# Optimization experiments

Measured on AMD Instinct MI355X. Metric: run time of the kernel, lower is better.

Reference implementation:

```python
import jax, jax.numpy as jnp
import numpy as np

N = 50000   # nodes
E = 600000  # edges per relation
H = 4       # heads
DH = 32     # head dim (out_feat // num_heads)
D = 128     # in_feat == out_feat
NEG_SLOPE = 0.2


def setup_inputs() -> dict:
    key = jax.random.key(0)
    ks = jax.random.split(key, 13)
    x = jax.random.normal(ks[0], (N, D), jnp.float32)
    src_r0 = jax.random.randint(ks[1], (E,), 0, N, jnp.int32)
    dst_r0 = jax.random.randint(ks[2], (E,), 0, N, jnp.int32)
    src_r1 = jax.random.randint(ks[3], (E,), 0, N, jnp.int32)
    dst_r1 = jax.random.randint(ks[4], (E,), 0, N, jnp.int32)
    s = 0.05  # keep activations moderate (xavier-like scale)
    W_r0 = jax.random.normal(ks[5], (D, H * DH), jnp.float32) * s
    attn_l_r0 = jax.random.normal(ks[6], (H, DH), jnp.float32) * s
    attn_r_r0 = jax.random.normal(ks[7], (H, DH), jnp.float32) * s
    W_r1 = jax.random.normal(ks[8], (D, H * DH), jnp.float32) * s
    attn_l_r1 = jax.random.normal(ks[9], (H, DH), jnp.float32) * s
    attn_r_r1 = jax.random.normal(ks[10], (H, DH), jnp.float32) * s
    loop_weight = jax.random.normal(ks[11], (D, D), jnp.float32) * s
    h_bias = jnp.zeros((D,), jnp.float32)
    return {"x": x, "src_r0": src_r0, "dst_r0": dst_r0, "src_r1": src_r1,
            "dst_r1": dst_r1, "W_r0": W_r0, "attn_l_r0": attn_l_r0,
            "attn_r_r0": attn_r_r0, "W_r1": W_r1, "attn_l_r1": attn_l_r1,
            "attn_r_r1": attn_r_r1, "loop_weight": loop_weight, "h_bias": h_bias}


def _gat_rel(x, src, dst, W, attn_l, attn_r):
    """DGL GATConv for one relation: fc -> per-node attn scalars -> edge
    leaky_relu -> per-dst softmax -> weighted scatter-sum. Heads flattened."""
    feat = (x @ W).reshape(-1, H, DH)                 # [N, H, DH]
    el = jnp.einsum('nhd,hd->nh', feat, attn_l)       # [N, H]
    er = jnp.einsum('nhd,hd->nh', feat, attn_r)       # [N, H]
    e = jax.nn.leaky_relu(el[src] + er[dst], NEG_SLOPE)  # [E, H]
    # edge softmax per destination node, per head (numerically stable)
    m = jax.ops.segment_max(e, dst, num_segments=N)   # [N, H]
    ex = jnp.exp(e - m[dst])                          # [E, H]
    z = jax.ops.segment_sum(ex, dst, num_segments=N)  # [N, H]
    a = ex / z[dst]                                   # [E, H]
    msg = a[:, :, None] * feat[src]                   # [E, H, DH]
    out = jax.ops.segment_sum(msg, dst, num_segments=N)  # [N, H, DH]
    return out.reshape(-1, H * DH)                    # [N, D] (concat heads)


def reference(x, src_r0, dst_r0, src_r1, dst_r1, W_r0, attn_l_r0, attn_r_r0,
              W_r1, attn_l_r1, attn_r_r1, loop_weight, h_bias):
    # HeteroGraphConv with default 'sum' aggregation across relations
    h = _gat_rel(x, src_r0, dst_r0, W_r0, attn_l_r0, attn_r_r0)
    h = h + _gat_rel(x, src_r1, dst_r1, W_r1, attn_l_r1, attn_r_r1)
    # self-loop linear + bias + activation (dropout p=0.0 is identity)
    h = h + x @ loop_weight + h_bias
    return jax.nn.relu(h)
```

## Files before the change

kernel.cpp:

```cpp
#include <hip/hip_runtime.h>
#include <math.h>


#define CAP 48
#define NB 256
#define BCAP 2752
#define BIN_EDGES 8192

typedef __attribute__((ext_vector_type(8))) short short8v;
typedef __attribute__((ext_vector_type(4))) float float4v;

__device__ __forceinline__ unsigned short f2bf(float f) {
  unsigned int u = __float_as_uint(f);
  unsigned int r = (u + 0x7fffu + ((u >> 16) & 1u)) >> 16;
  return (unsigned short)r;
}
__device__ __forceinline__ float2 bfpair(unsigned int u) {
  float2 r;
  r.x = __uint_as_float(u << 16);
  r.y = __uint_as_float(u & 0xffff0000u);
  return r;
}

__global__ __launch_bounds__(512) void prep_bin_kernel(
    const float* __restrict__ W0, const float* __restrict__ W1,
    const float* __restrict__ WL,
    const float* __restrict__ al0, const float* __restrict__ ar0,
    const float* __restrict__ al1, const float* __restrict__ ar1,
    const int* __restrict__ src0, const int* __restrict__ dst0,
    const int* __restrict__ src1, const int* __restrict__ dst1,
    unsigned short* __restrict__ Wtall,
    unsigned int* __restrict__ bpair, int* __restrict__ gcnt,
    int E, int width, int nconvb, int nbin)
{
  __shared__ int smem[512];
  const int t = threadIdx.x;

  if ((int)blockIdx.x < nconvb) {
    const int j = blockIdx.x * 512 + t;
    if (j < 4096) {
      const int rel = j >> 11;
      const int q = j & 2047;
      const int n = q >> 4;
      const int k0 = (q & 15) * 8;
      const float* W = rel ? W1 : W0;
      unsigned short o[8];
#pragma unroll
      for (int u = 0; u < 8; ++u) o[u] = f2bf(W[(size_t)(k0 + u) * 128 + n]);
      *(short8v*)&Wtall[(size_t)rel * 18432 + n * 128 + k0] = *(short8v*)o;
    } else if (j < 4352) {
      const int e = j - 4096;
      const int rel = e >> 7;
      const int q = e & 127;
      const int cIdx = q >> 4;
      const int isr = cIdx >> 2;
      const int h = cIdx & 3;
      const int k0 = (q & 15) * 8;
      const float* W = rel ? W1 : W0;
      const float* av = isr ? (rel ? ar1 : ar0) : (rel ? al1 : al0);
      unsigned short o[8];
#pragma unroll
      for (int u = 0; u < 8; ++u) {
        float s = 0.f;
#pragma unroll
        for (int d = 0; d < 32; ++d)
          s += W[(size_t)(k0 + u) * 128 + h * 32 + d] * av[h * 32 + d];
        o[u] = f2bf(s);
      }
      *(short8v*)&Wtall[(size_t)rel * 18432 + (128 + cIdx) * 128 + k0] = *(short8v*)o;
    } else if (j < 4608) {
      const int e = j - 4352;
      const int rel = e >> 7;
      const int q = e & 127;
      const int cIdx = 136 + (q >> 4);
      const int k0 = (q & 15) * 8;
      const short8v z = {0,0,0,0,0,0,0,0};
      *(short8v*)&Wtall[(size_t)rel * 18432 + cIdx * 128 + k0] = z;
    } else if (j < 6656) {
      const int e = j - 4608;
      const int n = e >> 4;
      const int k0 = (e & 15) * 8;
      unsigned short o[8];
#pragma unroll
      for (int u = 0; u < 8; ++u) o[u] = f2bf(WL[(size_t)(k0 + u) * 128 + n]);
      *(short8v*)&Wtall[(size_t)2 * 18432 + n * 128 + k0] = *(short8v*)o;
    }
  } else {
    int* cnt = smem;
    int* gb  = smem + NB;
    const int bid = blockIdx.x - nconvb;
    const int rel = (bid >= nbin) ? 1 : 0;
    const int ib  = rel ? (bid - nbin) : bid;
    const int* srcA = rel ? src1 : src0;
    const int* dstA = rel ? dst1 : dst0;
    const int base = ib * BIN_EDGES;
    const int cntE = min(E - base, BIN_EDGES);

    for (int i = t; i < NB; i += 512) cnt[i] = 0;
    __syncthreads();

    unsigned int epack[16]; int eb[16], epos[16];
#pragma unroll
    for (int q = 0; q < 16; ++q) {
      const int ei = q * 512 + t;
      if (ei < cntE) {
        const int s = srcA[base + ei];
        const int d = dstA[base + ei];
        const int b = d / width;
        const int ld = d - b * width;
        epack[q] = (unsigned int)s | ((unsigned int)ld << 16);
        eb[q] = b;
        epos[q] = atomicAdd(&cnt[b], 1);
      } else {
        eb[q] = -1;
      }
    }
    __syncthreads();
    for (int i = t; i < NB; i += 512)
      gb[i] = atomicAdd(&gcnt[rel * NB + i], cnt[i]);
    __syncthreads();
#pragma unroll
    for (int q = 0; q < 16; ++q) {
      if (eb[q] >= 0) {
        const int slot = gb[eb[q]] + epos[q];
        if (slot < BCAP)
          bpair[(size_t)(rel * NB + eb[q]) * BCAP + slot] = epack[q];
      }
    }
  }
}

__global__ __launch_bounds__(256) void gemm_ell_kernel(
    const float* __restrict__ x, const unsigned short* __restrict__ Wtall,
    unsigned short* __restrict__ f0, unsigned short* __restrict__ f1,
    unsigned short* __restrict__ xl,
    float* __restrict__ el0, float* __restrict__ er0,
    float* __restrict__ el1, float* __restrict__ er1,
    const unsigned int* __restrict__ bpair, const int* __restrict__ gcnt,
    int* __restrict__ deg, unsigned short* __restrict__ ell0,
    unsigned short* __restrict__ ell1,
    int N, int width, int ngemm)
{
  __shared__ int ldeg[256];

  if ((int)blockIdx.x < ngemm) {
    const int wave = threadIdx.x >> 6, lane = threadIdx.x & 63;
    const int lr = lane & 15, lk = lane >> 4;
    const int row0 = blockIdx.x * 128 + wave * 32;

    short8v a[2][4];
#pragma unroll
    for (int mf = 0; mf < 2; ++mf) {
      const int r = row0 + mf * 16 + lr;
#pragma unroll
      for (int kc = 0; kc < 4; ++kc) {
        if (r < N) {
          const float* xp = &x[(size_t)r * 128 + kc * 32 + lk * 8];
          float4 u = *(const float4*)xp;
          float4 v = *(const float4*)(xp + 4);
          unsigned short o[8];
          o[0]=f2bf(u.x); o[1]=f2bf(u.y); o[2]=f2bf(u.z); o[3]=f2bf(u.w);
          o[4]=f2bf(v.x); o[5]=f2bf(v.y); o[6]=f2bf(v.z); o[7]=f2bf(v.w);
          a[mf][kc] = *(short8v*)o;
        } else {
          a[mf][kc] = (short8v){0,0,0,0,0,0,0,0};
        }
      }
    }

#pragma unroll
    for (int w = 0; w < 3; ++w) {
      const unsigned short* Wp = Wtall + (size_t)w * 18432;
      const int NF = (w < 2) ? 9 : 8;
      float4v acc[2][9];
#pragma unroll
      for (int mf = 0; mf < 2; ++mf)
#pragma unroll
        for (int nf = 0; nf < 9; ++nf) acc[mf][nf] = (float4v){0.f, 0.f, 0.f, 0.f};
      for (int nf = 0; nf < NF; ++nf) {
        const unsigned short* Bp = &Wp[(size_t)(nf * 16 + lr) * 128];
#pragma unroll
        for (int kc = 0; kc < 4; ++kc) {
          const short8v b = *(const short8v*)&Bp[kc * 32 + lk * 8];
          acc[0][nf] = __builtin_amdgcn_mfma_f32_16x16x32_bf16(a[0][kc], b, acc[0][nf], 0, 0, 0);
          acc[1][nf] = __builtin_amdgcn_mfma_f32_16x16x32_bf16(a[1][kc], b, acc[1][nf], 0, 0, 0);
        }
      }

      unsigned short* dstp = (w == 0) ? f0 : (w == 1) ? f1 : xl;
#pragma unroll
      for (int mf = 0; mf < 2; ++mf) {
#pragma unroll
        for (int nf = 0; nf < 8; ++nf) {
          const int col = nf * 16 + lr;
#pragma unroll
          for (int j = 0; j < 4; ++j) {
            const int row = row0 + mf * 16 + lk * 4 + j;
            if (row < N) dstp[(size_t)row * 128 + col] = f2bf(acc[mf][nf][j]);
          }
        }
      }
      if (w < 2 && lr < 8) {
        float* ep = (lr < 4) ? (w ? el1 : el0) : (w ? er1 : er0);
        const int h = lr & 3;
#pragma unroll
        for (int mf = 0; mf < 2; ++mf)
#pragma unroll
          for (int j = 0; j < 4; ++j) {
            const int row = row0 + mf * 16 + lk * 4 + j;
            if (row < N) ep[row * 4 + h] = acc[mf][8][j];
          }
      }
    }
  } else {
    const int bid = blockIdx.x - ngemm;
    const int rel = bid >> 8;
    const int b = bid & 255;
    const int t = threadIdx.x;
    const int d0 = b * width;
    if (t < width) ldeg[t] = 0;
    __syncthreads();
    const int count = min(gcnt[rel * NB + b], BCAP);
    unsigned short* ell = rel ? ell1 : ell0;
    const unsigned int* bp = &bpair[(size_t)(rel * NB + b) * BCAP];
    for (int i = t; i < count; i += 256) {
      const unsigned int v = bp[i];
      const int src = (int)(v & 0xFFFFu);
      const int ld = (int)(v >> 16);
      const int slot = atomicAdd(&ldeg[ld], 1);
      if (slot < CAP) ell[(size_t)(d0 + ld) * CAP + slot] = (unsigned short)src;
    }
    __syncthreads();
    if (t < width && d0 + t < N) deg[rel * N + d0 + t] = ldeg[t];
  }
}

__global__ __launch_bounds__(256) void gat_aggregate_kernel(
    const unsigned short* __restrict__ f0, const unsigned short* __restrict__ f1,
    const unsigned short* __restrict__ xl,
    const float* __restrict__ el0, const float* __restrict__ er0,
    const float* __restrict__ el1, const float* __restrict__ er1,
    const int* __restrict__ deg,
    const unsigned short* __restrict__ ell0, const unsigned short* __restrict__ ell1,
    const float* __restrict__ bias, float* __restrict__ out, int N)
{
  __shared__ float p_lds[4][2][4][16];
  const int wid  = threadIdx.x >> 6;
  const int lane = threadIdx.x & 63;
  const int n = blockIdx.x * 4 + wid;
  if (n >= N) return;
  const int h  = lane >> 4;
  const int il = lane & 15;
  const int c  = lane * 2;

  const int rs0 = (int)ell0[(size_t)n * CAP + il];
  const int rs1 = (int)ell1[(size_t)n * CAP + il];
  const int d0 = min(deg[n], CAP);
  const int d1 = min(deg[N + n], CAP);
  const float er0h = er0[n * 4 + h];
  const float er1h = er1[n * 4 + h];

  const bool v0 = il < d0, v1 = il < d1;
  const int s0 = v0 ? rs0 : 0;
  const int s1 = v1 ? rs1 : 0;
  const float elv0 = el0[s0 * 4 + h];
  const float elv1 = el1[s1 * 4 + h];

  float m0, sum0, m1, sum1;
  {
    float e = elv0 + er0h;  e = e > 0.f ? e : 0.2f * e;
    float ev = v0 ? e : -INFINITY;
    float cm = ev;
    cm = fmaxf(cm, __shfl_xor(cm, 1)); cm = fmaxf(cm, __shfl_xor(cm, 2));
    cm = fmaxf(cm, __shfl_xor(cm, 4)); cm = fmaxf(cm, __shfl_xor(cm, 8));
    const float p = __expf(ev - cm);
    float cs = p;
    cs += __shfl_xor(cs, 1); cs += __shfl_xor(cs, 2);
    cs += __shfl_xor(cs, 4); cs += __shfl_xor(cs, 8);
    m0 = cm; sum0 = cs;
    p_lds[wid][0][h][il] = p;
  }
  {
    float e = elv1 + er1h;  e = e > 0.f ? e : 0.2f * e;
    float ev = v1 ? e : -INFINITY;
    float cm = ev;
    cm = fmaxf(cm, __shfl_xor(cm, 1)); cm = fmaxf(cm, __shfl_xor(cm, 2));
    cm = fmaxf(cm, __shfl_xor(cm, 4)); cm = fmaxf(cm, __shfl_xor(cm, 8));
    const float p = __expf(ev - cm);
    float cs = p;
    cs += __shfl_xor(cs, 1); cs += __shfl_xor(cs, 2);
    cs += __shfl_xor(cs, 4); cs += __shfl_xor(cs, 8);
    m1 = cm; sum1 = cs;
    p_lds[wid][1][h][il] = p;
  }

  unsigned int fu0[16], fu1[16];
#pragma unroll
  for (int i = 0; i < 16; ++i) {
    const int s = __builtin_amdgcn_readlane(s0, i);
    fu0[i] = *(const unsigned int*)&f0[(size_t)s * 128 + c];
  }
#pragma unroll
  for (int i = 0; i < 16; ++i) {
    const int s = __builtin_amdgcn_readlane(s1, i);
    fu1[i] = *(const unsigned int*)&f1[(size_t)s * 128 + c];
  }

  float ax0 = 0.f, ay0 = 0.f;
  {
    float p16[16];
    *(float4*)&p16[0]  = *(const float4*)&p_lds[wid][0][h][0];
    *(float4*)&p16[4]  = *(const float4*)&p_lds[wid][0][h][4];
    *(float4*)&p16[8]  = *(const float4*)&p_lds[wid][0][h][8];
    *(float4*)&p16[12] = *(const float4*)&p_lds[wid][0][h][12];
    float axa=0.f, aya=0.f, axb=0.f, ayb=0.f;
#pragma unroll
    for (int i = 0; i < 16; i += 2) {
      const float2 fa = bfpair(fu0[i]);
      const float2 fb2 = bfpair(fu0[i+1]);
      axa += p16[i]*fa.x;   aya += p16[i]*fa.y;
      axb += p16[i+1]*fb2.x; ayb += p16[i+1]*fb2.y;
    }
    ax0 = axa + axb; ay0 = aya + ayb;
  }
  float ax1 = 0.f, ay1 = 0.f;
  {
    float p16[16];
    *(float4*)&p16[0]  = *(const float4*)&p_lds[wid][1][h][0];
    *(float4*)&p16[4]  = *(const float4*)&p_lds[wid][1][h][4];
    *(float4*)&p16[8]  = *(const float4*)&p_lds[wid][1][h][8];
    *(float4*)&p16[12] = *(const float4*)&p_lds[wid][1][h][12];
    float axa=0.f, aya=0.f, axb=0.f, ayb=0.f;
#pragma unroll
    for (int i = 0; i < 16; i += 2) {
      const float2 fa = bfpair(fu1[i]);
      const float2 fb2 = bfpair(fu1[i+1]);
      axa += p16[i]*fa.x;   aya += p16[i]*fa.y;
      axb += p16[i+1]*fb2.x; ayb += p16[i+1]*fb2.y;
    }
    ax1 = axa + axb; ay1 = aya + ayb;
  }

  auto tail = [&](const unsigned short* ellp, const float* elp, float erh,
                  int d, const unsigned short* fbp, float& m, float& sum,
                  float& ax, float& ay, int slot) {
    for (int base = 16; base < d; base += 16) {
      const bool valid = (base + il) < d;
      int sv = (int)ellp[(size_t)n * CAP + base + il];
      sv = valid ? sv : 0;
      const float elv = elp[sv * 4 + h];
      float e = elv + erh; e = e > 0.f ? e : 0.2f * e;
      const float ev = valid ? e : -INFINITY;
      float cm = ev;
      cm = fmaxf(cm, __shfl_xor(cm, 1)); cm = fmaxf(cm, __shfl_xor(cm, 2));
      cm = fmaxf(cm, __shfl_xor(cm, 4)); cm = fmaxf(cm, __shfl_xor(cm, 8));
      const float mn = fmaxf(m, cm);
      const float scale = __expf(m - mn);
      const float p = __expf(ev - mn);
      float cs = p;
      cs += __shfl_xor(cs, 1); cs += __shfl_xor(cs, 2);
      cs += __shfl_xor(cs, 4); cs += __shfl_xor(cs, 8);
      sum = sum * scale + cs;
      m = mn;
      p_lds[wid][slot][h][il] = p;
      unsigned int fu[16];
#pragma unroll
      for (int i = 0; i < 16; ++i) {
        const int s = __builtin_amdgcn_readlane(sv, i);
        fu[i] = *(const unsigned int*)&fbp[(size_t)s * 128 + c];
      }
      float p16[16];
      *(float4*)&p16[0]  = *(const float4*)&p_lds[wid][slot][h][0];
      *(float4*)&p16[4]  = *(const float4*)&p_lds[wid][slot][h][4];
      *(float4*)&p16[8]  = *(const float4*)&p_lds[wid][slot][h][8];
      *(float4*)&p16[12] = *(const float4*)&p_lds[wid][slot][h][12];
      float axa=0.f, aya=0.f;
#pragma unroll
      for (int i = 0; i < 16; ++i) {
        const float2 f = bfpair(fu[i]);
        axa += p16[i]*f.x; aya += p16[i]*f.y;
      }
      ax = ax * scale + axa;
      ay = ay * scale + aya;
    }
  };
  if (d0 > 16) tail(ell0, el0, er0h, d0, f0, m0, sum0, ax0, ay0, 0);
  if (d1 > 16) tail(ell1, el1, er1h, d1, f1, m1, sum1, ax1, ay1, 1);

  float ox = 0.f, oy = 0.f;
  if (d0 > 0) { const float inv = 1.f / sum0; ox += ax0 * inv; oy += ay0 * inv; }
  if (d1 > 0) { const float inv = 1.f / sum1; ox += ax1 * inv; oy += ay1 * inv; }
  const float2 xlv = bfpair(*(const unsigned int*)&xl[(size_t)n * 128 + c]);
  const float2 bv  = *(const float2*)&bias[c];
  ox += xlv.x + bv.x;
  oy += xlv.y + bv.y;
  float2 res;
  res.x = fmaxf(ox, 0.f);
  res.y = fmaxf(oy, 0.f);
  *(float2*)&out[(size_t)n * 128 + c] = res;
}

extern "C" void kernel_launch(void* const* d_in, const int* in_sizes, int n_in,
                              void* d_out, int out_size, void* d_ws, size_t ws_size,
                              hipStream_t stream)
{
  const int N = in_sizes[0] / 128;
  const int E = in_sizes[1];

  const float* x    = (const float*)d_in[0];
  const int* src0   = (const int*)d_in[1];
  const int* dst0   = (const int*)d_in[2];
  const int* src1   = (const int*)d_in[3];
  const int* dst1   = (const int*)d_in[4];
  const float* W0   = (const float*)d_in[5];
  const float* al0  = (const float*)d_in[6];
  const float* ar0  = (const float*)d_in[7];
  const float* W1   = (const float*)d_in[8];
  const float* al1  = (const float*)d_in[9];
  const float* ar1  = (const float*)d_in[10];
  const float* WL   = (const float*)d_in[11];
  const float* bias = (const float*)d_in[12];
  float* out = (float*)d_out;

  char* p = (char*)d_ws;
  auto alloc = [&](size_t bytes) { char* r = p; p += (bytes + 255) & ~(size_t)255; return r; };
  unsigned short* f0 = (unsigned short*)alloc((size_t)N * 128 * 2);
  unsigned short* f1 = (unsigned short*)alloc((size_t)N * 128 * 2);
  unsigned short* xl = (unsigned short*)alloc((size_t)N * 128 * 2);
  float* el0 = (float*)alloc((size_t)N * 4 * 4);
  float* er0 = (float*)alloc((size_t)N * 4 * 4);
  float* el1 = (float*)alloc((size_t)N * 4 * 4);
  float* er1 = (float*)alloc((size_t)N * 4 * 4);
  int* deg   = (int*)alloc((size_t)2 * N * 4);
  unsigned short* ell0 = (unsigned short*)alloc((size_t)CAP * N * 2);
  unsigned short* ell1 = (unsigned short*)alloc((size_t)CAP * N * 2);
  unsigned int* bpair = (unsigned int*)alloc((size_t)2 * NB * BCAP * 4);
  int* gcnt  = (int*)alloc((size_t)2 * NB * 4);
  unsigned short* Wtall = (unsigned short*)alloc((size_t)(2 * 144 + 128) * 128 * 2);

  const int width = (N + NB - 1) / NB;
  const int ngemm = (N + 127) / 128;
  const int nbin  = (E + BIN_EDGES - 1) / BIN_EDGES;
  const int nconvb = 13;

  hipMemsetAsync(gcnt, 0, (size_t)2 * NB * 4, stream);

  prep_bin_kernel<<<nconvb + 2 * nbin, 512, 0, stream>>>(
      W0, W1, WL, al0, ar0, al1, ar1, src0, dst0, src1, dst1,
      Wtall, bpair, gcnt, E, width, nconvb, nbin);

  gemm_ell_kernel<<<ngemm + 2 * NB, 256, 0, stream>>>(
      x, Wtall, f0, f1, xl, el0, er0, el1, er1,
      bpair, gcnt, deg, ell0, ell1, N, width, ngemm);

  gat_aggregate_kernel<<<(N + 3) / 4, 256, 0, stream>>>(
      f0, f1, xl, el0, er0, el1, er1, deg, ell0, ell1, bias, out, N);
}
```

Before: 128.9 us.

## Co-schedule edge binning with GEMM, split ELL build, two nodes per wave

```diff
diff --git a/kernel.cpp b/kernel.cpp
--- a/kernel.cpp
+++ b/kernel.cpp
@@ -5,7 +5,7 @@
 #define CAP 48
 #define NB 256
 #define BCAP 2752
-#define BIN_EDGES 8192
+#define BIN_EDGES 4096
 
 typedef __attribute__((ext_vector_type(8))) short short8v;
 typedef __attribute__((ext_vector_type(4))) float float4v;
@@ -22,126 +22,80 @@
   return r;
 }
 
-__global__ __launch_bounds__(512) void prep_bin_kernel(
+__global__ __launch_bounds__(256) void prep_kernel(
     const float* __restrict__ W0, const float* __restrict__ W1,
     const float* __restrict__ WL,
     const float* __restrict__ al0, const float* __restrict__ ar0,
     const float* __restrict__ al1, const float* __restrict__ ar1,
+    unsigned short* __restrict__ Wtall, int* __restrict__ gcnt)
+{
+  const int t = threadIdx.x;
+  if (blockIdx.x == 0) {
+    gcnt[t] = 0;
+    gcnt[t + 256] = 0;
+  }
+  const int j = blockIdx.x * 256 + t;
+  if (j < 4096) {
+    const int rel = j >> 11;
+    const int q = j & 2047;
+    const int n = q >> 4;
+    const int k0 = (q & 15) * 8;
+    const float* W = rel ? W1 : W0;
+    unsigned short o[8];
+#pragma unroll
+    for (int u = 0; u < 8; ++u) o[u] = f2bf(W[(size_t)(k0 + u) * 128 + n]);
+    *(short8v*)&Wtall[(size_t)rel * 18432 + n * 128 + k0] = *(short8v*)o;
+  } else if (j < 4352) {
+    const int e = j - 4096;
+    const int rel = e >> 7;
+    const int q = e & 127;
+    const int cIdx = q >> 4;
+    const int isr = cIdx >> 2;
+    const int h = cIdx & 3;
+    const int k0 = (q & 15) * 8;
+    const float* W = rel ? W1 : W0;
+    const float* av = isr ? (rel ? ar1 : ar0) : (rel ? al1 : al0);
+    unsigned short o[8];
+#pragma unroll
+    for (int u = 0; u < 8; ++u) {
+      float s = 0.f;
+#pragma unroll
+      for (int d = 0; d < 32; ++d)
+        s += W[(size_t)(k0 + u) * 128 + h * 32 + d] * av[h * 32 + d];
+      o[u] = f2bf(s);
+    }
+    *(short8v*)&Wtall[(size_t)rel * 18432 + (128 + cIdx) * 128 + k0] = *(short8v*)o;
+  } else if (j < 4608) {
+    const int e = j - 4352;
+    const int rel = e >> 7;
+    const int q = e & 127;
+    const int cIdx = 136 + (q >> 4);
+    const int k0 = (q & 15) * 8;
+    const short8v z = {0,0,0,0,0,0,0,0};
+    *(short8v*)&Wtall[(size_t)rel * 18432 + cIdx * 128 + k0] = z;
+  } else if (j < 6656) {
+    const int e = j - 4608;
+    const int n = e >> 4;
+    const int k0 = (e & 15) * 8;
+    unsigned short o[8];
+#pragma unroll
+    for (int u = 0; u < 8; ++u) o[u] = f2bf(WL[(size_t)(k0 + u) * 128 + n]);
+    *(short8v*)&Wtall[(size_t)2 * 18432 + n * 128 + k0] = *(short8v*)o;
+  }
+}
+
+__global__ __launch_bounds__(256) void gemm_bin_kernel(
+    const float* __restrict__ x, const unsigned short* __restrict__ Wtall,
     const int* __restrict__ src0, const int* __restrict__ dst0,
     const int* __restrict__ src1, const int* __restrict__ dst1,
-    unsigned short* __restrict__ Wtall,
-    unsigned int* __restrict__ bpair, int* __restrict__ gcnt,
-    int E, int width, int nconvb, int nbin)
-{
-  __shared__ int smem[512];
-  const int t = threadIdx.x;
-
-  if ((int)blockIdx.x < nconvb) {
-    const int j = blockIdx.x * 512 + t;
-    if (j < 4096) {
-      const int rel = j >> 11;
-      const int q = j & 2047;
-      const int n = q >> 4;
-      const int k0 = (q & 15) * 8;
-      const float* W = rel ? W1 : W0;
-      unsigned short o[8];
-#pragma unroll
-      for (int u = 0; u < 8; ++u) o[u] = f2bf(W[(size_t)(k0 + u) * 128 + n]);
-      *(short8v*)&Wtall[(size_t)rel * 18432 + n * 128 + k0] = *(short8v*)o;
-    } else if (j < 4352) {
-      const int e = j - 4096;
-      const int rel = e >> 7;
-      const int q = e & 127;
-      const int cIdx = q >> 4;
-      const int isr = cIdx >> 2;
-      const int h = cIdx & 3;
-      const int k0 = (q & 15) * 8;
-      const float* W = rel ? W1 : W0;
-      const float* av = isr ? (rel ? ar1 : ar0) : (rel ? al1 : al0);
-      unsigned short o[8];
-#pragma unroll
-      for (int u = 0; u < 8; ++u) {
-        float s = 0.f;
-#pragma unroll
-        for (int d = 0; d < 32; ++d)
-          s += W[(size_t)(k0 + u) * 128 + h * 32 + d] * av[h * 32 + d];
-        o[u] = f2bf(s);
-      }
-      *(short8v*)&Wtall[(size_t)rel * 18432 + (128 + cIdx) * 128 + k0] = *(short8v*)o;
-    } else if (j < 4608) {
-      const int e = j - 4352;
-      const int rel = e >> 7;
-      const int q = e & 127;
-      const int cIdx = 136 + (q >> 4);
-      const int k0 = (q & 15) * 8;
-      const short8v z = {0,0,0,0,0,0,0,0};
-      *(short8v*)&Wtall[(size_t)rel * 18432 + cIdx * 128 + k0] = z;
-    } else if (j < 6656) {
-      const int e = j - 4608;
-      const int n = e >> 4;
-      const int k0 = (e & 15) * 8;
-      unsigned short o[8];
-#pragma unroll
-      for (int u = 0; u < 8; ++u) o[u] = f2bf(WL[(size_t)(k0 + u) * 128 + n]);
-      *(short8v*)&Wtall[(size_t)2 * 18432 + n * 128 + k0] = *(short8v*)o;
-    }
-  } else {
-    int* cnt = smem;
-    int* gb  = smem + NB;
-    const int bid = blockIdx.x - nconvb;
-    const int rel = (bid >= nbin) ? 1 : 0;
-    const int ib  = rel ? (bid - nbin) : bid;
-    const int* srcA = rel ? src1 : src0;
-    const int* dstA = rel ? dst1 : dst0;
-    const int base = ib * BIN_EDGES;
-    const int cntE = min(E - base, BIN_EDGES);
-
-    for (int i = t; i < NB; i += 512) cnt[i] = 0;
-    __syncthreads();
-
-    unsigned int epack[16]; int eb[16], epos[16];
-#pragma unroll
-    for (int q = 0; q < 16; ++q) {
-      const int ei = q * 512 + t;
-      if (ei < cntE) {
-        const int s = srcA[base + ei];
-        const int d = dstA[base + ei];
-        const int b = d / width;
-        const int ld = d - b * width;
-        epack[q] = (unsigned int)s | ((unsigned int)ld << 16);
-        eb[q] = b;
-        epos[q] = atomicAdd(&cnt[b], 1);
-      } else {
-        eb[q] = -1;
-      }
-    }
-    __syncthreads();
-    for (int i = t; i < NB; i += 512)
-      gb[i] = atomicAdd(&gcnt[rel * NB + i], cnt[i]);
-    __syncthreads();
-#pragma unroll
-    for (int q = 0; q < 16; ++q) {
-      if (eb[q] >= 0) {
-        const int slot = gb[eb[q]] + epos[q];
-        if (slot < BCAP)
-          bpair[(size_t)(rel * NB + eb[q]) * BCAP + slot] = epack[q];
-      }
-    }
-  }
-}
-
-__global__ __launch_bounds__(256) void gemm_ell_kernel(
-    const float* __restrict__ x, const unsigned short* __restrict__ Wtall,
     unsigned short* __restrict__ f0, unsigned short* __restrict__ f1,
     unsigned short* __restrict__ xl,
     float* __restrict__ el0, float* __restrict__ er0,
     float* __restrict__ el1, float* __restrict__ er1,
-    const unsigned int* __restrict__ bpair, const int* __restrict__ gcnt,
-    int* __restrict__ deg, unsigned short* __restrict__ ell0,
-    unsigned short* __restrict__ ell1,
-    int N, int width, int ngemm)
+    unsigned int* __restrict__ bpair, int* __restrict__ gcnt,
+    int N, int E, int width, int ngemm, int nbin)
 {
-  __shared__ int ldeg[256];
+  __shared__ int smem[512];
 
   if ((int)blockIdx.x < ngemm) {
     const int wave = threadIdx.x >> 6, lane = threadIdx.x & 63;
@@ -213,26 +167,74 @@
       }
     }
   } else {
+    int* cnt = smem;
+    int* gb  = smem + NB;
+    const int t = threadIdx.x;
     const int bid = blockIdx.x - ngemm;
-    const int rel = bid >> 8;
-    const int b = bid & 255;
-    const int t = threadIdx.x;
-    const int d0 = b * width;
-    if (t < width) ldeg[t] = 0;
+    const int rel = (bid >= nbin) ? 1 : 0;
+    const int ib  = rel ? (bid - nbin) : bid;
+    const int* srcA = rel ? src1 : src0;
+    const int* dstA = rel ? dst1 : dst0;
+    const int base = ib * BIN_EDGES;
+    const int cntE = min(E - base, BIN_EDGES);
+
+    cnt[t] = 0;
     __syncthreads();
-    const int count = min(gcnt[rel * NB + b], BCAP);
-    unsigned short* ell = rel ? ell1 : ell0;
-    const unsigned int* bp = &bpair[(size_t)(rel * NB + b) * BCAP];
-    for (int i = t; i < count; i += 256) {
-      const unsigned int v = bp[i];
-      const int src = (int)(v & 0xFFFFu);
-      const int ld = (int)(v >> 16);
-      const int slot = atomicAdd(&ldeg[ld], 1);
-      if (slot < CAP) ell[(size_t)(d0 + ld) * CAP + slot] = (unsigned short)src;
+
+    unsigned int epack[16]; int eb[16], epos[16];
+#pragma unroll
+    for (int q = 0; q < 16; ++q) {
+      const int ei = q * 256 + t;
+      if (ei < cntE) {
+        const int s = srcA[base + ei];
+        const int d = dstA[base + ei];
+        const int b = d / width;
+        const int ld = d - b * width;
+        epack[q] = (unsigned int)s | ((unsigned int)ld << 16);
+        eb[q] = b;
+        epos[q] = atomicAdd(&cnt[b], 1);
+      } else {
+        eb[q] = -1;
+      }
     }
     __syncthreads();
-    if (t < width && d0 + t < N) deg[rel * N + d0 + t] = ldeg[t];
+    gb[t] = atomicAdd(&gcnt[rel * NB + t], cnt[t]);
+    __syncthreads();
+#pragma unroll
+    for (int q = 0; q < 16; ++q) {
+      if (eb[q] >= 0) {
+        const int slot = gb[eb[q]] + epos[q];
+        if (slot < BCAP)
+          bpair[(size_t)(rel * NB + eb[q]) * BCAP + slot] = epack[q];
+      }
+    }
   }
+}
+
+__global__ __launch_bounds__(256) void ell_build_kernel(
+    const unsigned int* __restrict__ bpair, const int* __restrict__ gcnt,
+    int* __restrict__ deg, unsigned short* __restrict__ ell0,
+    unsigned short* __restrict__ ell1, int N, int width)
+{
+  __shared__ int ldeg[256];
+  const int rel = blockIdx.x >> 8;
+  const int b = blockIdx.x & 255;
+  const int t = threadIdx.x;
+  const int d0 = b * width;
+  if (t < width) ldeg[t] = 0;
+  __syncthreads();
+  const int count = min(gcnt[rel * NB + b], BCAP);
+  unsigned short* ell = rel ? ell1 : ell0;
+  const unsigned int* bp = &bpair[(size_t)(rel * NB + b) * BCAP];
+  for (int i = t; i < count; i += 256) {
+    const unsigned int v = bp[i];
+    const int src = (int)(v & 0xFFFFu);
+    const int ld = (int)(v >> 16);
+    const int slot = atomicAdd(&ldeg[ld], 1);
+    if (slot < CAP) ell[(size_t)(d0 + ld) * CAP + slot] = (unsigned short)src;
+  }
+  __syncthreads();
+  if (t < width && d0 + t < N) deg[rel * N + d0 + t] = ldeg[t];
 }
 
 __global__ __launch_bounds__(256) void gat_aggregate_kernel(
@@ -247,157 +249,171 @@
   __shared__ float p_lds[4][2][4][16];
   const int wid  = threadIdx.x >> 6;
   const int lane = threadIdx.x & 63;
-  const int n = blockIdx.x * 4 + wid;
-  if (n >= N) return;
   const int h  = lane >> 4;
   const int il = lane & 15;
   const int c  = lane * 2;
-
-  const int rs0 = (int)ell0[(size_t)n * CAP + il];
-  const int rs1 = (int)ell1[(size_t)n * CAP + il];
-  const int d0 = min(deg[n], CAP);
-  const int d1 = min(deg[N + n], CAP);
-  const float er0h = er0[n * 4 + h];
-  const float er1h = er1[n * 4 + h];
-
-  const bool v0 = il < d0, v1 = il < d1;
-  const int s0 = v0 ? rs0 : 0;
-  const int s1 = v1 ? rs1 : 0;
-  const float elv0 = el0[s0 * 4 + h];
-  const float elv1 = el1[s1 * 4 + h];
-
-  float m0, sum0, m1, sum1;
-  {
-    float e = elv0 + er0h;  e = e > 0.f ? e : 0.2f * e;
-    float ev = v0 ? e : -INFINITY;
-    float cm = ev;
-    cm = fmaxf(cm, __shfl_xor(cm, 1)); cm = fmaxf(cm, __shfl_xor(cm, 2));
-    cm = fmaxf(cm, __shfl_xor(cm, 4)); cm = fmaxf(cm, __shfl_xor(cm, 8));
-    const float p = __expf(ev - cm);
-    float cs = p;
-    cs += __shfl_xor(cs, 1); cs += __shfl_xor(cs, 2);
-    cs += __shfl_xor(cs, 4); cs += __shfl_xor(cs, 8);
-    m0 = cm; sum0 = cs;
-    p_lds[wid][0][h][il] = p;
-  }
-  {
-    float e = elv1 + er1h;  e = e > 0.f ? e : 0.2f * e;
-    float ev = v1 ? e : -INFINITY;
-    float cm = ev;
-    cm = fmaxf(cm, __shfl_xor(cm, 1)); cm = fmaxf(cm, __shfl_xor(cm, 2));
-    cm = fmaxf(cm, __shfl_xor(cm, 4)); cm = fmaxf(cm, __shfl_xor(cm, 8));
-    const float p = __expf(ev - cm);
-    float cs = p;
-    cs += __shfl_xor(cs, 1); cs += __shfl_xor(cs, 2);
-    cs += __shfl_xor(cs, 4); cs += __shfl_xor(cs, 8);
-    m1 = cm; sum1 = cs;
-    p_lds[wid][1][h][il] = p;
-  }
-
-  unsigned int fu0[16], fu1[16];
-#pragma unroll
-  for (int i = 0; i < 16; ++i) {
-    const int s = __builtin_amdgcn_readlane(s0, i);
-    fu0[i] = *(const unsigned int*)&f0[(size_t)s * 128 + c];
-  }
-#pragma unroll
-  for (int i = 0; i < 16; ++i) {
-    const int s = __builtin_amdgcn_readlane(s1, i);
-    fu1[i] = *(const unsigned int*)&f1[(size_t)s * 128 + c];
-  }
-
-  float ax0 = 0.f, ay0 = 0.f;
-  {
-    float p16[16];
-    *(float4*)&p16[0]  = *(const float4*)&p_lds[wid][0][h][0];
-    *(float4*)&p16[4]  = *(const float4*)&p_lds[wid][0][h][4];
-    *(float4*)&p16[8]  = *(const float4*)&p_lds[wid][0][h][8];
-    *(float4*)&p16[12] = *(const float4*)&p_lds[wid][0][h][12];
-    float axa=0.f, aya=0.f, axb=0.f, ayb=0.f;
-#pragma unroll
-    for (int i = 0; i < 16; i += 2) {
-      const float2 fa = bfpair(fu0[i]);
-      const float2 fb2 = bfpair(fu0[i+1]);
-      axa += p16[i]*fa.x;   aya += p16[i]*fa.y;
-      axb += p16[i+1]*fb2.x; ayb += p16[i+1]*fb2.y;
-    }
-    ax0 = axa + axb; ay0 = aya + ayb;
-  }
-  float ax1 = 0.f, ay1 = 0.f;
-  {
-    float p16[16];
-    *(float4*)&p16[0]  = *(const float4*)&p_lds[wid][1][h][0];
-    *(float4*)&p16[4]  = *(const float4*)&p_lds[wid][1][h][4];
-    *(float4*)&p16[8]  = *(const float4*)&p_lds[wid][1][h][8];
-    *(float4*)&p16[12] = *(const float4*)&p_lds[wid][1][h][12];
-    float axa=0.f, aya=0.f, axb=0.f, ayb=0.f;
-#pragma unroll
-    for (int i = 0; i < 16; i += 2) {
-      const float2 fa = bfpair(fu1[i]);
-      const float2 fb2 = bfpair(fu1[i+1]);
-      axa += p16[i]*fa.x;   aya += p16[i]*fa.y;
-      axb += p16[i+1]*fb2.x; ayb += p16[i+1]*fb2.y;
-    }
-    ax1 = axa + axb; ay1 = aya + ayb;
-  }
-
-  auto tail = [&](const unsigned short* ellp, const float* elp, float erh,
-                  int d, const unsigned short* fbp, float& m, float& sum,
-                  float& ax, float& ay, int slot) {
-    for (int base = 16; base < d; base += 16) {
-      const bool valid = (base + il) < d;
-      int sv = (int)ellp[(size_t)n * CAP + base + il];
-      sv = valid ? sv : 0;
-      const float elv = elp[sv * 4 + h];
-      float e = elv + erh; e = e > 0.f ? e : 0.2f * e;
-      const float ev = valid ? e : -INFINITY;
+  const int n0 = (blockIdx.x * 4 + wid) * 2;
+  if (n0 >= N) return;
+  const bool actB = (n0 + 1) < N;
+  const int nA = n0, nB = actB ? (n0 + 1) : n0;
+
+  const int rA0 = (int)ell0[(size_t)nA * CAP + il];
+  const int rA1 = (int)ell1[(size_t)nA * CAP + il];
+  const int rB0 = (int)ell0[(size_t)nB * CAP + il];
+  const int rB1 = (int)ell1[(size_t)nB * CAP + il];
+  const int dA0 = min(deg[nA], CAP),     dA1 = min(deg[N + nA], CAP);
+  const int dB0 = actB ? min(deg[nB], CAP) : 0;
+  const int dB1 = actB ? min(deg[N + nB], CAP) : 0;
+  const float erA0 = er0[nA * 4 + h], erA1 = er1[nA * 4 + h];
+  const float erB0 = er0[nB * 4 + h], erB1 = er1[nB * 4 + h];
+
+  const int sA0 = (il < dA0) ? rA0 : 0;
+  const int sA1 = (il < dA1) ? rA1 : 0;
+  const int sB0 = (il < dB0) ? rB0 : 0;
+  const int sB1 = (il < dB1) ? rB1 : 0;
+
+  const float elA0 = el0[sA0 * 4 + h];
+  const float elA1 = el1[sA1 * 4 + h];
+  const float elB0 = el0[sB0 * 4 + h];
+  const float elB1 = el1[sB1 * 4 + h];
+
+  auto process = [&](int n, int s0, int s1, int d0, int d1,
+                     float er0h, float er1h, float elv0, float elv1) {
+    float m0, sum0, m1, sum1;
+    {
+      float e = elv0 + er0h;  e = e > 0.f ? e : 0.2f * e;
+      float ev = (il < d0) ? e : -INFINITY;
       float cm = ev;
       cm = fmaxf(cm, __shfl_xor(cm, 1)); cm = fmaxf(cm, __shfl_xor(cm, 2));
       cm = fmaxf(cm, __shfl_xor(cm, 4)); cm = fmaxf(cm, __shfl_xor(cm, 8));
-      const float mn = fmaxf(m, cm);
-      const float scale = __expf(m - mn);
-      const float p = __expf(ev - mn);
+      const float p = __expf(ev - cm);
       float cs = p;
       cs += __shfl_xor(cs, 1); cs += __shfl_xor(cs, 2);
       cs += __shfl_xor(cs, 4); cs += __shfl_xor(cs, 8);
-      sum = sum * scale + cs;
-      m = mn;
-      p_lds[wid][slot][h][il] = p;
-      unsigned int fu[16];
-#pragma unroll
-      for (int i = 0; i < 16; ++i) {
-        const int s = __builtin_amdgcn_readlane(sv, i);
-        fu[i] = *(const unsigned int*)&fbp[(size_t)s * 128 + c];
-      }
+      m0 = cm; sum0 = cs;
+      p_lds[wid][0][h][il] = p;
+    }
+    {
+      float e = elv1 + er1h;  e = e > 0.f ? e : 0.2f * e;
+      float ev = (il < d1) ? e : -INFINITY;
+      float cm = ev;
+      cm = fmaxf(cm, __shfl_xor(cm, 1)); cm = fmaxf(cm, __shfl_xor(cm, 2));
+      cm = fmaxf(cm, __shfl_xor(cm, 4)); cm = fmaxf(cm, __shfl_xor(cm, 8));
+      const float p = __expf(ev - cm);
+      float cs = p;
+      cs += __shfl_xor(cs, 1); cs += __shfl_xor(cs, 2);
+      cs += __shfl_xor(cs, 4); cs += __shfl_xor(cs, 8);
+      m1 = cm; sum1 = cs;
+      p_lds[wid][1][h][il] = p;
+    }
+
+    unsigned int fu0[16], fu1[16];
+#pragma unroll
+    for (int i = 0; i < 16; ++i) {
+      const int s = __builtin_amdgcn_readlane(s0, i);
+      fu0[i] = *(const unsigned int*)&f0[(size_t)s * 128 + c];
+    }
+#pragma unroll
+    for (int i = 0; i < 16; ++i) {
+      const int s = __builtin_amdgcn_readlane(s1, i);
+      fu1[i] = *(const unsigned int*)&f1[(size_t)s * 128 + c];
+    }
+
+    float ax0, ay0, ax1, ay1;
+    {
       float p16[16];
-      *(float4*)&p16[0]  = *(const float4*)&p_lds[wid][slot][h][0];
-      *(float4*)&p16[4]  = *(const float4*)&p_lds[wid][slot][h][4];
-      *(float4*)&p16[8]  = *(const float4*)&p_lds[wid][slot][h][8];
-      *(float4*)&p16[12] = *(const float4*)&p_lds[wid][slot][h][12];
-      float axa=0.f, aya=0.f;
-#pragma unroll
-      for (int i = 0; i < 16; ++i) {
-        const float2 f = bfpair(fu[i]);
-        axa += p16[i]*f.x; aya += p16[i]*f.y;
-      }
-      ax = ax * scale + axa;
-      ay = ay * scale + aya;
-    }
+      *(float4*)&p16[0]  = *(const float4*)&p_lds[wid][0][h][0];
+      *(float4*)&p16[4]  = *(const float4*)&p_lds[wid][0][h][4];
+      *(float4*)&p16[8]  = *(const float4*)&p_lds[wid][0][h][8];
+      *(float4*)&p16[12] = *(const float4*)&p_lds[wid][0][h][12];
+      float axa=0.f, aya=0.f, axb=0.f, ayb=0.f;
+#pragma unroll
+      for (int i = 0; i < 16; i += 2) {
+        const float2 fa = bfpair(fu0[i]);
+        const float2 fb2 = bfpair(fu0[i+1]);
+        axa += p16[i]*fa.x;   aya += p16[i]*fa.y;
+        axb += p16[i+1]*fb2.x; ayb += p16[i+1]*fb2.y;
+      }
+      ax0 = axa + axb; ay0 = aya + ayb;
+    }
+    {
+      float p16[16];
+      *(float4*)&p16[0]  = *(const float4*)&p_lds[wid][1][h][0];
+      *(float4*)&p16[4]  = *(const float4*)&p_lds[wid][1][h][4];
+      *(float4*)&p16[8]  = *(const float4*)&p_lds[wid][1][h][8];
+      *(float4*)&p16[12] = *(const float4*)&p_lds[wid][1][h][12];
+      float axa=0.f, aya=0.f, axb=0.f, ayb=0.f;
+#pragma unroll
+      for (int i = 0; i < 16; i += 2) {
+        const float2 fa = bfpair(fu1[i]);
+        const float2 fb2 = bfpair(fu1[i+1]);
+        axa += p16[i]*fa.x;   aya += p16[i]*fa.y;
+        axb += p16[i+1]*fb2.x; ayb += p16[i+1]*fb2.y;
+      }
+      ax1 = axa + axb; ay1 = aya + ayb;
+    }
+
+    auto tail = [&](const unsigned short* ellp, const float* elp, float erh,
+                    int d, const unsigned short* fbp, float& m, float& sum,
+                    float& ax, float& ay, int slot) {
+      for (int base = 16; base < d; base += 16) {
+        const bool valid = (base + il) < d;
+        int sv = (int)ellp[(size_t)n * CAP + base + il];
+        sv = valid ? sv : 0;
+        const float elv = elp[sv * 4 + h];
+        float e = elv + erh; e = e > 0.f ? e : 0.2f * e;
+        const float ev = valid ? e : -INFINITY;
+        float cm = ev;
+        cm = fmaxf(cm, __shfl_xor(cm, 1)); cm = fmaxf(cm, __shfl_xor(cm, 2));
+        cm = fmaxf(cm, __shfl_xor(cm, 4)); cm = fmaxf(cm, __shfl_xor(cm, 8));
+        const float mn = fmaxf(m, cm);
+        const float scale = __expf(m - mn);
+        const float p = __expf(ev - mn);
+        float cs = p;
+        cs += __shfl_xor(cs, 1); cs += __shfl_xor(cs, 2);
+        cs += __shfl_xor(cs, 4); cs += __shfl_xor(cs, 8);
+        sum = sum * scale + cs;
+        m = mn;
+        p_lds[wid][slot][h][il] = p;
+        unsigned int fu[16];
+#pragma unroll
+        for (int i = 0; i < 16; ++i) {
+          const int s = __builtin_amdgcn_readlane(sv, i);
+          fu[i] = *(const unsigned int*)&fbp[(size_t)s * 128 + c];
+        }
+        float p16[16];
+        *(float4*)&p16[0]  = *(const float4*)&p_lds[wid][slot][h][0];
+        *(float4*)&p16[4]  = *(const float4*)&p_lds[wid][slot][h][4];
+        *(float4*)&p16[8]  = *(const float4*)&p_lds[wid][slot][h][8];
+        *(float4*)&p16[12] = *(const float4*)&p_lds[wid][slot][h][12];
+        float axa=0.f, aya=0.f;
+#pragma unroll
+        for (int i = 0; i < 16; ++i) {
+          const float2 f = bfpair(fu[i]);
+          axa += p16[i]*f.x; aya += p16[i]*f.y;
+        }
+        ax = ax * scale + axa;
+        ay = ay * scale + aya;
+      }
+    };
+    if (d0 > 16) tail(ell0, el0, er0h, d0, f0, m0, sum0, ax0, ay0, 0);
+    if (d1 > 16) tail(ell1, el1, er1h, d1, f1, m1, sum1, ax1, ay1, 1);
+
+    float ox = 0.f, oy = 0.f;
+    if (d0 > 0) { const float inv = 1.f / sum0; ox += ax0 * inv; oy += ay0 * inv; }
+    if (d1 > 0) { const float inv = 1.f / sum1; ox += ax1 * inv; oy += ay1 * inv; }
+    const float2 xlv = bfpair(*(const unsigned int*)&xl[(size_t)n * 128 + c]);
+    const float2 bv  = *(const float2*)&bias[c];
+    ox += xlv.x + bv.x;
+    oy += xlv.y + bv.y;
+    float2 res;
+    res.x = fmaxf(ox, 0.f);
+    res.y = fmaxf(oy, 0.f);
+    *(float2*)&out[(size_t)n * 128 + c] = res;
   };
-  if (d0 > 16) tail(ell0, el0, er0h, d0, f0, m0, sum0, ax0, ay0, 0);
-  if (d1 > 16) tail(ell1, el1, er1h, d1, f1, m1, sum1, ax1, ay1, 1);
-
-  float ox = 0.f, oy = 0.f;
-  if (d0 > 0) { const float inv = 1.f / sum0; ox += ax0 * inv; oy += ay0 * inv; }
-  if (d1 > 0) { const float inv = 1.f / sum1; ox += ax1 * inv; oy += ay1 * inv; }
-  const float2 xlv = bfpair(*(const unsigned int*)&xl[(size_t)n * 128 + c]);
-  const float2 bv  = *(const float2*)&bias[c];
-  ox += xlv.x + bv.x;
-  oy += xlv.y + bv.y;
-  float2 res;
-  res.x = fmaxf(ox, 0.f);
-  res.y = fmaxf(oy, 0.f);
-  *(float2*)&out[(size_t)n * 128 + c] = res;
+
+  process(nA, sA0, sA1, dA0, dA1, erA0, erA1, elA0, elA1);
+  if (actB) process(nB, sB0, sB1, dB0, dB1, erB0, erB1, elB0, elB1);
 }
 
 extern "C" void kernel_launch(void* const* d_in, const int* in_sizes, int n_in,
@@ -441,18 +457,17 @@
   const int width = (N + NB - 1) / NB;
   const int ngemm = (N + 127) / 128;
   const int nbin  = (E + BIN_EDGES - 1) / BIN_EDGES;
-  const int nconvb = 13;
-
-  hipMemsetAsync(gcnt, 0, (size_t)2 * NB * 4, stream);
-
-  prep_bin_kernel<<<nconvb + 2 * nbin, 512, 0, stream>>>(
-      W0, W1, WL, al0, ar0, al1, ar1, src0, dst0, src1, dst1,
-      Wtall, bpair, gcnt, E, width, nconvb, nbin);
-
-  gemm_ell_kernel<<<ngemm + 2 * NB, 256, 0, stream>>>(
-      x, Wtall, f0, f1, xl, el0, er0, el1, er1,
-      bpair, gcnt, deg, ell0, ell1, N, width, ngemm);
-
-  gat_aggregate_kernel<<<(N + 3) / 4, 256, 0, stream>>>(
+
+  prep_kernel<<<26, 256, 0, stream>>>(
+      W0, W1, WL, al0, ar0, al1, ar1, Wtall, gcnt);
+
+  gemm_bin_kernel<<<ngemm + 2 * nbin, 256, 0, stream>>>(
+      x, Wtall, src0, dst0, src1, dst1,
+      f0, f1, xl, el0, er0, el1, er1, bpair, gcnt, N, E, width, ngemm, nbin);
+
+  ell_build_kernel<<<2 * NB, 256, 0, stream>>>(
+      bpair, gcnt, deg, ell0, ell1, N, width);
+
+  gat_aggregate_kernel<<<((N + 1) / 2 + 3) / 4, 256, 0, stream>>>(
       f0, f1, xl, el0, er0, el1, er1, deg, ell0, ell1, bias, out, N);
 }
```

Measured after the change: 132.4 us. 1.03x slower.

## Split prep and binning kernels, fold gcnt reset, hoist feature gathers

Applied to the files above, without the earlier changes.

```diff
diff --git a/kernel.cpp b/kernel.cpp
--- a/kernel.cpp
+++ b/kernel.cpp
@@ -5,7 +5,7 @@
 #define CAP 48
 #define NB 256
 #define BCAP 2752
-#define BIN_EDGES 8192
+#define BIN_EDGES 4096
 
 typedef __attribute__((ext_vector_type(8))) short short8v;
 typedef __attribute__((ext_vector_type(4))) float float4v;
@@ -22,110 +22,114 @@
   return r;
 }
 
-__global__ __launch_bounds__(512) void prep_bin_kernel(
+__global__ __launch_bounds__(256) void prep_kernel(
     const float* __restrict__ W0, const float* __restrict__ W1,
     const float* __restrict__ WL,
     const float* __restrict__ al0, const float* __restrict__ ar0,
     const float* __restrict__ al1, const float* __restrict__ ar1,
+    unsigned short* __restrict__ Wtall, int* __restrict__ gcnt)
+{
+  const int t = threadIdx.x;
+  if (blockIdx.x == 0) {
+    gcnt[t] = 0;
+    gcnt[t + 256] = 0;
+  }
+  const int j = blockIdx.x * 256 + t;
+  if (j < 4096) {
+    const int rel = j >> 11;
+    const int q = j & 2047;
+    const int n = q >> 4;
+    const int k0 = (q & 15) * 8;
+    const float* W = rel ? W1 : W0;
+    unsigned short o[8];
+#pragma unroll
+    for (int u = 0; u < 8; ++u) o[u] = f2bf(W[(size_t)(k0 + u) * 128 + n]);
+    *(short8v*)&Wtall[(size_t)rel * 18432 + n * 128 + k0] = *(short8v*)o;
+  } else if (j < 4352) {
+    const int e = j - 4096;
+    const int rel = e >> 7;
+    const int q = e & 127;
+    const int cIdx = q >> 4;
+    const int isr = cIdx >> 2;
+    const int h = cIdx & 3;
+    const int k0 = (q & 15) * 8;
+    const float* W = rel ? W1 : W0;
+    const float* av = isr ? (rel ? ar1 : ar0) : (rel ? al1 : al0);
+    unsigned short o[8];
+#pragma unroll
+    for (int u = 0; u < 8; ++u) {
+      float s = 0.f;
+#pragma unroll
+      for (int d = 0; d < 32; ++d)
+        s += W[(size_t)(k0 + u) * 128 + h * 32 + d] * av[h * 32 + d];
+      o[u] = f2bf(s);
+    }
+    *(short8v*)&Wtall[(size_t)rel * 18432 + (128 + cIdx) * 128 + k0] = *(short8v*)o;
+  } else if (j < 4608) {
+    const int e = j - 4352;
+    const int rel = e >> 7;
+    const int q = e & 127;
+    const int cIdx = 136 + (q >> 4);
+    const int k0 = (q & 15) * 8;
+    const short8v z = {0,0,0,0,0,0,0,0};
+    *(short8v*)&Wtall[(size_t)rel * 18432 + cIdx * 128 + k0] = z;
+  } else if (j < 6656) {
+    const int e = j - 4608;
+    const int n = e >> 4;
+    const int k0 = (e & 15) * 8;
+    unsigned short o[8];
+#pragma unroll
+    for (int u = 0; u < 8; ++u) o[u] = f2bf(WL[(size_t)(k0 + u) * 128 + n]);
+    *(short8v*)&Wtall[(size_t)2 * 18432 + n * 128 + k0] = *(short8v*)o;
+  }
+}
+
+__global__ __launch_bounds__(256) void bin_kernel(
     const int* __restrict__ src0, const int* __restrict__ dst0,
     const int* __restrict__ src1, const int* __restrict__ dst1,
-    unsigned short* __restrict__ Wtall,
     unsigned int* __restrict__ bpair, int* __restrict__ gcnt,
-    int E, int width, int nconvb, int nbin)
+    int E, int width, int nbin)
 {
   __shared__ int smem[512];
+  int* cnt = smem;
+  int* gb  = smem + NB;
   const int t = threadIdx.x;
-
-  if ((int)blockIdx.x < nconvb) {
-    const int j = blockIdx.x * 512 + t;
-    if (j < 4096) {
-      const int rel = j >> 11;
-      const int q = j & 2047;
-      const int n = q >> 4;
-      const int k0 = (q & 15) * 8;
-      const float* W = rel ? W1 : W0;
-      unsigned short o[8];
-#pragma unroll
-      for (int u = 0; u < 8; ++u) o[u] = f2bf(W[(size_t)(k0 + u) * 128 + n]);
-      *(short8v*)&Wtall[(size_t)rel * 18432 + n * 128 + k0] = *(short8v*)o;
-    } else if (j < 4352) {
-      const int e = j - 4096;
-      const int rel = e >> 7;
-      const int q = e & 127;
-      const int cIdx = q >> 4;
-      const int isr = cIdx >> 2;
-      const int h = cIdx & 3;
-      const int k0 = (q & 15) * 8;
-      const float* W = rel ? W1 : W0;
-      const float* av = isr ? (rel ? ar1 : ar0) : (rel ? al1 : al0);
-      unsigned short o[8];
-#pragma unroll
-      for (int u = 0; u < 8; ++u) {
-        float s = 0.f;
-#pragma unroll
-        for (int d = 0; d < 32; ++d)
-          s += W[(size_t)(k0 + u) * 128 + h * 32 + d] * av[h * 32 + d];
-        o[u] = f2bf(s);
-      }
-      *(short8v*)&Wtall[(size_t)rel * 18432 + (128 + cIdx) * 128 + k0] = *(short8v*)o;
-    } else if (j < 4608) {
-      const int e = j - 4352;
-      const int rel = e >> 7;
-      const int q = e & 127;
-      const int cIdx = 136 + (q >> 4);
-      const int k0 = (q & 15) * 8;
-      const short8v z = {0,0,0,0,0,0,0,0};
-      *(short8v*)&Wtall[(size_t)rel * 18432 + cIdx * 128 + k0] = z;
-    } else if (j < 6656) {
-      const int e = j - 4608;
-      const int n = e >> 4;
-      const int k0 = (e & 15) * 8;
-      unsigned short o[8];
-#pragma unroll
-      for (int u = 0; u < 8; ++u) o[u] = f2bf(WL[(size_t)(k0 + u) * 128 + n]);
-      *(short8v*)&Wtall[(size_t)2 * 18432 + n * 128 + k0] = *(short8v*)o;
-    }
-  } else {
-    int* cnt = smem;
-    int* gb  = smem + NB;
-    const int bid = blockIdx.x - nconvb;
-    const int rel = (bid >= nbin) ? 1 : 0;
-    const int ib  = rel ? (bid - nbin) : bid;
-    const int* srcA = rel ? src1 : src0;
-    const int* dstA = rel ? dst1 : dst0;
-    const int base = ib * BIN_EDGES;
-    const int cntE = min(E - base, BIN_EDGES);
-
-    for (int i = t; i < NB; i += 512) cnt[i] = 0;
-    __syncthreads();
-
-    unsigned int epack[16]; int eb[16], epos[16];
-#pragma unroll
-    for (int q = 0; q < 16; ++q) {
-      const int ei = q * 512 + t;
-      if (ei < cntE) {
-        const int s = srcA[base + ei];
-        const int d = dstA[base + ei];
-        const int b = d / width;
-        const int ld = d - b * width;
-        epack[q] = (unsigned int)s | ((unsigned int)ld << 16);
-        eb[q] = b;
-        epos[q] = atomicAdd(&cnt[b], 1);
-      } else {
-        eb[q] = -1;
-      }
-    }
-    __syncthreads();
-    for (int i = t; i < NB; i += 512)
-      gb[i] = atomicAdd(&gcnt[rel * NB + i], cnt[i]);
-    __syncthreads();
-#pragma unroll
-    for (int q = 0; q < 16; ++q) {
-      if (eb[q] >= 0) {
-        const int slot = gb[eb[q]] + epos[q];
-        if (slot < BCAP)
-          bpair[(size_t)(rel * NB + eb[q]) * BCAP + slot] = epack[q];
-      }
+  const int bid = blockIdx.x;
+  const int rel = (bid >= nbin) ? 1 : 0;
+  const int ib  = rel ? (bid - nbin) : bid;
+  const int* srcA = rel ? src1 : src0;
+  const int* dstA = rel ? dst1 : dst0;
+  const int base = ib * BIN_EDGES;
+  const int cntE = min(E - base, BIN_EDGES);
+
+  cnt[t] = 0;
+  __syncthreads();
+
+  unsigned int epack[16]; int eb[16], epos[16];
+#pragma unroll
+  for (int q = 0; q < 16; ++q) {
+    const int ei = q * 256 + t;
+    if (ei < cntE) {
+      const int s = srcA[base + ei];
+      const int d = dstA[base + ei];
+      const int b = d / width;
+      const int ld = d - b * width;
+      epack[q] = (unsigned int)s | ((unsigned int)ld << 16);
+      eb[q] = b;
+      epos[q] = atomicAdd(&cnt[b], 1);
+    } else {
+      eb[q] = -1;
+    }
+  }
+  __syncthreads();
+  gb[t] = atomicAdd(&gcnt[rel * NB + t], cnt[t]);
+  __syncthreads();
+#pragma unroll
+  for (int q = 0; q < 16; ++q) {
+    if (eb[q] >= 0) {
+      const int slot = gb[eb[q]] + epos[q];
+      if (slot < BCAP)
+        bpair[(size_t)(rel * NB + eb[q]) * BCAP + slot] = epack[q];
     }
   }
 }
@@ -263,8 +267,21 @@
   const bool v0 = il < d0, v1 = il < d1;
   const int s0 = v0 ? rs0 : 0;
   const int s1 = v1 ? rs1 : 0;
+
   const float elv0 = el0[s0 * 4 + h];
   const float elv1 = el1[s1 * 4 + h];
+
+  unsigned int fu0[16], fu1[16];
+#pragma unroll
+  for (int i = 0; i < 16; ++i) {
+    const int s = __builtin_amdgcn_readlane(s0, i);
+    fu0[i] = *(const unsigned int*)&f0[(size_t)s * 128 + c];
+  }
+#pragma unroll
+  for (int i = 0; i < 16; ++i) {
+    const int s = __builtin_amdgcn_readlane(s1, i);
+    fu1[i] = *(const unsigned int*)&f1[(size_t)s * 128 + c];
+  }
 
   float m0, sum0, m1, sum1;
   {
@@ -294,18 +311,6 @@
     p_lds[wid][1][h][il] = p;
   }
 
-  unsigned int fu0[16], fu1[16];
-#pragma unroll
-  for (int i = 0; i < 16; ++i) {
-    const int s = __builtin_amdgcn_readlane(s0, i);
-    fu0[i] = *(const unsigned int*)&f0[(size_t)s * 128 + c];
-  }
-#pragma unroll
-  for (int i = 0; i < 16; ++i) {
-    const int s = __builtin_amdgcn_readlane(s1, i);
-    fu1[i] = *(const unsigned int*)&f1[(size_t)s * 128 + c];
-  }
-
   float ax0 = 0.f, ay0 = 0.f;
   {
     float p16[16];
@@ -349,6 +354,12 @@
       int sv = (int)ellp[(size_t)n * CAP + base + il];
       sv = valid ? sv : 0;
       const float elv = elp[sv * 4 + h];
+      unsigned int fu[16];
+#pragma unroll
+      for (int i = 0; i < 16; ++i) {
+        const int s = __builtin_amdgcn_readlane(sv, i);
+        fu[i] = *(const unsigned int*)&fbp[(size_t)s * 128 + c];
+      }
       float e = elv + erh; e = e > 0.f ? e : 0.2f * e;
       const float ev = valid ? e : -INFINITY;
       float cm = ev;
@@ -363,12 +374,6 @@
       sum = sum * scale + cs;
       m = mn;
       p_lds[wid][slot][h][il] = p;
-      unsigned int fu[16];
-#pragma unroll
-      for (int i = 0; i < 16; ++i) {
-        const int s = __builtin_amdgcn_readlane(sv, i);
-        fu[i] = *(const unsigned int*)&fbp[(size_t)s * 128 + c];
-      }
       float p16[16];
       *(float4*)&p16[0]  = *(const float4*)&p_lds[wid][slot][h][0];
       *(float4*)&p16[4]  = *(const float4*)&p_lds[wid][slot][h][4];
@@ -441,13 +446,12 @@
   const int width = (N + NB - 1) / NB;
   const int ngemm = (N + 127) / 128;
   const int nbin  = (E + BIN_EDGES - 1) / BIN_EDGES;
-  const int nconvb = 13;
-
-  hipMemsetAsync(gcnt, 0, (size_t)2 * NB * 4, stream);
-
-  prep_bin_kernel<<<nconvb + 2 * nbin, 512, 0, stream>>>(
-      W0, W1, WL, al0, ar0, al1, ar1, src0, dst0, src1, dst1,
-      Wtall, bpair, gcnt, E, width, nconvb, nbin);
+
+  prep_kernel<<<26, 256, 0, stream>>>(
+      W0, W1, WL, al0, ar0, al1, ar1, Wtall, gcnt);
+
+  bin_kernel<<<2 * nbin, 256, 0, stream>>>(
+      src0, dst0, src1, dst1, bpair, gcnt, E, width, nbin);
 
   gemm_ell_kernel<<<ngemm + 2 * NB, 256, 0, stream>>>(
       x, Wtall, f0, f1, xl, el0, er0, el1, er1,
```

After: 138.8 us. 1.08x slower.
